# Performance work log

Measured on AMD Instinct MI355X. Metric: run time of the kernel, lower is better.

Reference implementation:

```python
import jax, jax.numpy as jnp
import numpy as np

HIDDEN = 2048
NUM_HEADS = 16
HEAD_SIZE = HIDDEN // NUM_HEADS  # 128
SEQ = 2048
BATCH = 2


def alibi_causal_bias(seq_len: int, num_heads: int) -> jnp.ndarray:
    """[1, H, S, S] bias: -(i-j)*slope for j<=i, -inf for j>i (per source mask)."""
    i = jnp.arange(seq_len)[:, None]
    j = jnp.arange(seq_len)[None, :]
    dist = -(i - j).astype(jnp.float32)            # 0 on diag, -(i-j) below
    causal = jnp.where(j > i, -jnp.inf, 0.0)
    base = jnp.where(j > i, 0.0, dist) + causal     # [S, S]
    if num_heads <= 8:
        slopes = jnp.asarray([1.0 / 2**k for k in range(num_heads)], jnp.float32)
    else:
        slopes = jnp.asarray([1.0 / 2**(k / 2) for k in range(num_heads)], jnp.float32)
    # NOTE: source multiplies the mask (including -inf part) by the slope;
    # -inf * positive slope is still -inf, so applying slopes to the finite
    # part and adding -inf causal term is equivalent.
    return slopes[None, :, None, None] * dist[None, None] * (j <= i)[None, None] + causal[None, None]


def setup_inputs() -> dict:
    key = jax.random.key(0)
    ks = jax.random.split(key, 3)
    sd = 1.0 / np.sqrt(HIDDEN)
    return {
        "x": jax.random.normal(ks[0], (BATCH, SEQ, HIDDEN), jnp.float32),
        "Wqkv": jax.random.normal(ks[1], (HIDDEN, 3 * HIDDEN), jnp.float32) * sd,
        "bqkv": jnp.zeros((3 * HIDDEN,), jnp.float32),
        "Wo": jax.random.normal(ks[2], (HIDDEN, HIDDEN), jnp.float32) * sd,
        "bo": jnp.zeros((HIDDEN,), jnp.float32),
    }


def reference(x, Wqkv, bqkv, Wo, bo):
    b, s, h = x.shape
    scale = 1.0 / np.sqrt(HEAD_SIZE)
    qkv = x @ Wqkv + bqkv                                   # [b, s, 3h]
    q, k, v = jnp.split(qkv, 3, axis=-1)
    def heads(t):
        return t.reshape(b, s, NUM_HEADS, HEAD_SIZE).transpose(0, 2, 1, 3)
    q, k, v = heads(q), heads(k), heads(v)                  # [b, H, s, d]
    scores = jnp.einsum("bhid,bhjd->bhij", q, k) * scale
    scores = scores + alibi_causal_bias(s, NUM_HEADS)
    attn = jax.nn.softmax(scores, axis=-1)                  # dropout=0 (eval)
    out = jnp.einsum("bhij,bhjd->bhid", attn, v)            # [b, H, s, d]
    out = out.transpose(0, 2, 1, 3).reshape(b, s, NUM_HEADS * HEAD_SIZE)
    return out @ Wo + bo
```

## Files before the change

kernel.cpp:

```cpp
#include <hip/hip_runtime.h>

typedef __attribute__((ext_vector_type(4))) float f32x4;
typedef __attribute__((ext_vector_type(8))) __bf16 bf16x8;
typedef unsigned short u16;

#define GAS(p) ((const __attribute__((address_space(1))) void*)(p))
#define LAS(p) ((__attribute__((address_space(3))) void*)(p))

__device__ __forceinline__ u16 f32_to_bf16(float f) {
  unsigned u = __builtin_bit_cast(unsigned, f);
  u += 0x7FFFu + ((u >> 16) & 1u);
  return (u16)(u >> 16);
}

__global__ __launch_bounds__(256) void k_convert(const float* __restrict__ X,
                                                 u16* __restrict__ Y, int n4) {
  int i = blockIdx.x * 256 + threadIdx.x;
  if (i >= n4) return;
  float4 v = ((const float4*)X)[i];
  ushort4 r;
  r.x = f32_to_bf16(v.x); r.y = f32_to_bf16(v.y);
  r.z = f32_to_bf16(v.z); r.w = f32_to_bf16(v.w);
  ((ushort4*)Y)[i] = r;
}

__global__ __launch_bounds__(256) void k_transpose_w(const float* __restrict__ W,
                                                     u16* __restrict__ WT,
                                                     int K, int N) {
  __shared__ float tile[32][33];
  int n0 = blockIdx.x * 32, k0 = blockIdx.y * 32;
  int tx = threadIdx.x & 31, ty = threadIdx.x >> 5;
#pragma unroll
  for (int r = 0; r < 4; ++r)
    tile[ty + r * 8][tx] = W[(long)(k0 + ty + r * 8) * N + n0 + tx];
  __syncthreads();
#pragma unroll
  for (int r = 0; r < 4; ++r)
    WT[(long)(n0 + ty + r * 8) * K + k0 + tx] = f32_to_bf16(tile[tx][ty + r * 8]);
}

__global__ __launch_bounds__(256) void k_transpose_v(const u16* __restrict__ V,
                                                     u16* __restrict__ VT) {
  __shared__ u16 tile[32][34];
  int s0 = blockIdx.x * 32, d0 = blockIdx.y * 32, bh = blockIdx.z;
  int tx = threadIdx.x & 31, ty = threadIdx.x >> 5;
  const u16* Vb = V + (long)bh * 2048 * 128;
  u16* VTb = VT + (long)bh * 128 * 2048;
#pragma unroll
  for (int r = 0; r < 4; ++r)
    tile[ty + r * 8][tx] = Vb[(long)(s0 + ty + r * 8) * 128 + d0 + tx];
  __syncthreads();
#pragma unroll
  for (int r = 0; r < 4; ++r)
    VTb[(long)(d0 + ty + r * 8) * 2048 + s0 + tx] = tile[tx][ty + r * 8];
}

template <int EPI>
__global__ __launch_bounds__(512, 2) void k_gemm(
    const u16* __restrict__ A, const u16* __restrict__ BT,
    const float* __restrict__ bias,
    u16* __restrict__ Qo, u16* __restrict__ Ko, u16* __restrict__ Vo,
    float* __restrict__ Cout, int M, int N, int K) {
  __shared__ alignas(16) u16 AS[3][128 * 64];
  __shared__ alignas(16) u16 BS[3][256 * 64];
  const int wave = threadIdx.x >> 6, lane = threadIdx.x & 63;
  const int wr = wave >> 2, wc = wave & 3;
  const int l15 = lane & 15, l4 = lane >> 4;
  const int sl = lane & 7, sr = (lane >> 3) & 7;

  const int nwg = gridDim.x;
  const int swz = ((int)blockIdx.x & 7) * (nwg >> 3) + ((int)blockIdx.x >> 3);
  const int mt = M >> 7;
  const int bm = swz % mt, bn = swz / mt;
  const int brow = bm * 128, bcol = bn * 256;
  const int NT = K >> 6;

  const u16* aBase = A + (long)(brow + wave * 8 + sr) * K + (sl ^ sr) * 8;
  const u16* bBase = BT + (long)(bcol + wave * 8 + sr) * K + (sl ^ sr) * 8;
  const long K64 = (long)K * 64;

  auto stage = [&](int t, int buf) {
    const long t64 = (long)t * 64;
#pragma unroll
    for (int j = 0; j < 2; ++j)
      __builtin_amdgcn_global_load_lds(GAS(aBase + t64 + j * K64),
                                       LAS(&AS[buf][(wave + j * 8) * 512]), 16, 0, 0);
#pragma unroll
    for (int j = 0; j < 4; ++j)
      __builtin_amdgcn_global_load_lds(GAS(bBase + t64 + j * K64),
                                       LAS(&BS[buf][(wave + j * 8) * 512]), 16, 0, 0);
  };

  const f32x4 fzero = {0.f, 0.f, 0.f, 0.f};
  f32x4 acc[4][4];
#pragma unroll
  for (int m = 0; m < 4; ++m)
#pragma unroll
    for (int n = 0; n < 4; ++n) acc[m][n] = fzero;

  auto compute = [&](int buf) {
    const u16* Ac = &AS[buf][0];
    const u16* Bc = &BS[buf][0];
    bf16x8 afr[4][2], bfr[4][2];
#pragma unroll
    for (int f = 0; f < 4; ++f)
#pragma unroll
      for (int kk = 0; kk < 2; ++kk) {
        const int Ra = wr * 64 + f * 16 + l15;
        afr[f][kk] =
            *(const bf16x8*)(Ac + Ra * 64 + (((kk * 4 + l4) ^ (l15 & 7)) * 8));
        const int Rb = wc * 64 + f * 16 + l15;
        bfr[f][kk] =
            *(const bf16x8*)(Bc + Rb * 64 + (((kk * 4 + l4) ^ (l15 & 7)) * 8));
      }
    __builtin_amdgcn_s_setprio(1);
#pragma unroll
    for (int m = 0; m < 4; ++m)
#pragma unroll
      for (int n = 0; n < 4; ++n)
#pragma unroll
        for (int kk = 0; kk < 2; ++kk)
          acc[m][n] = __builtin_amdgcn_mfma_f32_16x16x32_bf16(
              afr[m][kk], bfr[n][kk], acc[m][n], 0, 0, 0);
    __builtin_amdgcn_s_setprio(0);
  };

  stage(0, 0);
  stage(1, 1);
  int bufc = 0;
  for (int t = 0; t < NT - 1; ++t) {
    asm volatile("s_waitcnt vmcnt(6)" ::: "memory");
    __builtin_amdgcn_s_barrier();
    if (t + 2 < NT) {
      int bufn = bufc + 2;
      if (bufn >= 3) bufn -= 3;
      stage(t + 2, bufn);
    }
    compute(bufc);
    ++bufc;
    if (bufc == 3) bufc = 0;
  }
  asm volatile("s_waitcnt vmcnt(0)" ::: "memory");
  __builtin_amdgcn_s_barrier();
  compute(bufc);

  if (EPI == 0) {
#pragma unroll
    for (int n = 0; n < 4; ++n) {
      const int col = bcol + wc * 64 + n * 16 + l15;
      const int which = col >> 11;
      u16* dst = (which == 0) ? Qo : (which == 1) ? Ko : Vo;
      const int cc = col & 2047;
      const int h = cc >> 7, d = cc & 127;
      const float bv = bias[col];
#pragma unroll
      for (int m = 0; m < 4; ++m) {
#pragma unroll
        for (int r = 0; r < 4; ++r) {
          const int row = brow + wr * 64 + m * 16 + l4 * 4 + r;
          const int bb = row >> 11, s = row & 2047;
          dst[(((long)(bb * 16 + h)) * 2048 + s) * 128 + d] =
              f32_to_bf16(acc[m][n][r] + bv);
        }
      }
    }
  } else {
#pragma unroll
    for (int m = 0; m < 4; ++m)
#pragma unroll
      for (int r = 0; r < 4; ++r) {
        const int row = brow + wr * 64 + m * 16 + l4 * 4 + r;
#pragma unroll
        for (int n = 0; n < 4; ++n) {
          const int col = bcol + wc * 64 + n * 16 + l15;
          Cout[(long)row * N + col] = acc[m][n][r] + bias[col];
        }
      }
  }
}

__global__ __launch_bounds__(256, 4) void k_attn(const u16* __restrict__ Q,
                                                 const u16* __restrict__ Kp,
                                                 const u16* __restrict__ VT,
                                                 u16* __restrict__ Oa) {
  __shared__ alignas(16) u16 Kl[2][64 * 128];
  __shared__ alignas(16) u16 Vl[2][128 * 64];
  __shared__ alignas(16) u16 Pl[4][16 * 64];
  const int b = blockIdx.x;
  const int bh = b & 31;
  const int qt = 31 - (b >> 5);
  const int bb = bh >> 4, h = bh & 15;
  const int wave = threadIdx.x >> 6, lane = threadIdx.x & 63;
  const int l15 = lane & 15, l4 = lane >> 4;
  const int l7 = lane & 7, l8 = lane >> 3;
  const float LOG2E = 1.4426950408889634f;
  const float scale = 0.08838834764831845f * LOG2E;
  const float slope = exp2f(-0.5f * (float)h) * LOG2E;

  const int q0 = qt * 64 + wave * 16;
  const u16* Qb = Q + ((long)bh * 2048 + q0 + l15) * 128;
  bf16x8 qf[4];
#pragma unroll
  for (int kk = 0; kk < 4; ++kk) qf[kk] = *(const bf16x8*)(Qb + kk * 32 + l4 * 8);

  const u16* Kb = Kp + (long)bh * 2048 * 128;
  const u16* VTb = VT + (long)bh * 128 * 2048;

  auto stageK = [&](int jt, int buf) {
#pragma unroll
    for (int g = 0; g < 4; ++g) {
      const int wcc = g * 4 + wave;
      const int row = wcc * 4 + l4;
      const u16* src = Kb + (long)(jt * 64 + row) * 128 + ((l15 ^ (row & 7)) * 8);
      __builtin_amdgcn_global_load_lds(GAS(src), LAS(&Kl[buf][wcc * 512]), 16, 0, 0);
    }
  };
  auto stageV = [&](int jt, int buf) {
#pragma unroll
    for (int g = 0; g < 4; ++g) {
      const int wcc = g * 4 + wave;
      const int d = wcc * 8 + l8;
      const u16* src = VTb + (long)d * 2048 + jt * 64 + ((l7 ^ l8) * 8);
      __builtin_amdgcn_global_load_lds(GAS(src), LAS(&Vl[buf][wcc * 512]), 16, 0, 0);
    }
  };

  float rs[4];
  f32x4 O[8];
  const f32x4 fzero = {0.f, 0.f, 0.f, 0.f};
#pragma unroll
  for (int r = 0; r < 4; ++r) rs[r] = 0.f;
#pragma unroll
  for (int nb = 0; nb < 8; ++nb) O[nb] = fzero;

  u16* Pw = Pl[wave];
  const int irow = q0 + l4 * 4;
  const int sw = l15 & 7;

  stageK(0, 0);
  stageV(0, 0);
  __syncthreads();

  for (int jt = 0; jt <= qt; ++jt) {
    const int cur = jt & 1;
    if (jt < qt) {
      stageK(jt + 1, cur ^ 1);
      stageV(jt + 1, cur ^ 1);
    }
    const u16* Kc = Kl[cur];
    const u16* Vc = Vl[cur];
    const int j0 = jt * 64;
#pragma unroll
    for (int cb = 0; cb < 4; ++cb) {
      f32x4 sa = fzero;
      const u16* kp = Kc + (cb * 16 + l15) * 128;
#pragma unroll
      for (int kk = 0; kk < 4; ++kk) {
        bf16x8 kf = *(const bf16x8*)(kp + (((kk * 4 + l4) ^ sw) * 8));
        sa = __builtin_amdgcn_mfma_f32_16x16x32_bf16(qf[kk], kf, sa, 0, 0, 0);
      }
      const int j = j0 + cb * 16 + l15;
#pragma unroll
      for (int r = 0; r < 4; ++r) {
        int i = irow + r;
        float s = sa[r] * scale - slope * (float)(i - j);
        float p = __builtin_amdgcn_exp2f((j <= i) ? s : -1e30f);
        rs[r] += p;
        int rloc = l4 * 4 + r;
        int cbyte = (cb * 16 + l15) * 2;
        *(u16*)((char*)Pw + rloc * 128 + (cbyte ^ ((rloc & 7) << 4))) =
            f32_to_bf16(p);
      }
    }
    bf16x8 pf0 = *(const bf16x8*)((char*)Pw + l15 * 128 +
                                  ((l4 * 16) ^ ((l15 & 7) << 4)));
    bf16x8 pf1 = *(const bf16x8*)((char*)Pw + l15 * 128 +
                                  ((64 + l4 * 16) ^ ((l15 & 7) << 4)));
#pragma unroll
    for (int nb = 0; nb < 8; ++nb) {
      const u16* vp = Vc + (nb * 16 + l15) * 64;
      bf16x8 v0 = *(const bf16x8*)(vp + ((l4 ^ sw) * 8));
      bf16x8 v1 = *(const bf16x8*)(vp + (((4 + l4) ^ sw) * 8));
      O[nb] = __builtin_amdgcn_mfma_f32_16x16x32_bf16(pf0, v0, O[nb], 0, 0, 0);
      O[nb] = __builtin_amdgcn_mfma_f32_16x16x32_bf16(pf1, v1, O[nb], 0, 0, 0);
    }
    __syncthreads();
  }
#pragma unroll
  for (int r = 0; r < 4; ++r) {
    float v = rs[r];
    v += __shfl_xor(v, 1);
    v += __shfl_xor(v, 2);
    v += __shfl_xor(v, 4);
    v += __shfl_xor(v, 8);
    float inv = 1.f / v;
    int i = irow + r;
    u16* op = Oa + ((long)bb * 2048 + i) * 2048 + h * 128;
#pragma unroll
    for (int nb = 0; nb < 8; ++nb) op[nb * 16 + l15] = f32_to_bf16(O[nb][r] * inv);
  }
}

extern "C" void kernel_launch(void* const* d_in, const int* in_sizes, int n_in,
                              void* d_out, int out_size, void* d_ws, size_t ws_size,
                              hipStream_t stream) {
  const float* x = (const float*)d_in[0];
  const float* Wqkv = (const float*)d_in[1];
  const float* bqkv = (const float*)d_in[2];
  const float* Wo = (const float*)d_in[3];
  const float* bo = (const float*)d_in[4];
  float* out = (float*)d_out;

  char* ws = (char*)d_ws;
  u16* xb = (u16*)(ws);
  u16* VTb = (u16*)(ws);
  u16* WqkvT = (u16*)(ws + 16777216);
  u16* attn_out = (u16*)(ws + 16777216);
  u16* WoT = (u16*)(ws + 16777216 + 25165824);
  u16* Qb = (u16*)(ws + 50331648);
  u16* Kb = (u16*)(ws + 67108864);
  u16* Vb = (u16*)(ws + 83886080);

  k_convert<<<8192, 256, 0, stream>>>(x, xb, 8388608 / 4);
  k_transpose_w<<<dim3(192, 64), 256, 0, stream>>>(Wqkv, WqkvT, 2048, 6144);
  k_transpose_w<<<dim3(64, 64), 256, 0, stream>>>(Wo, WoT, 2048, 2048);
  k_gemm<0><<<dim3(768), 512, 0, stream>>>(xb, WqkvT, bqkv, Qb, Kb, Vb,
                                           nullptr, 4096, 6144, 2048);
  k_transpose_v<<<dim3(64, 4, 32), 256, 0, stream>>>(Vb, VTb);
  k_attn<<<dim3(1024), 256, 0, stream>>>(Qb, Kb, VTb, attn_out);
  k_gemm<1><<<dim3(256), 512, 0, stream>>>(attn_out, WoT, bo, nullptr,
                                           nullptr, nullptr, out, 4096, 2048,
                                           2048);
}
```

Measured before the change: 292.2 us.

## Use 256x256 tiled GEMM with interleaved load/compute schedule for QKV projection

```diff
diff --git a/kernel.cpp b/kernel.cpp
--- a/kernel.cpp
+++ b/kernel.cpp
@@ -53,6 +53,179 @@
 #pragma unroll
   for (int r = 0; r < 4; ++r)
     VTb[(long)(d0 + ty + r * 8) * 2048 + s0 + tx] = tile[tx][ty + r * 8];
+}
+
+template <int EPI>
+__global__ __launch_bounds__(512, 2) void k_gemm256(
+    const u16* __restrict__ A, const u16* __restrict__ BT,
+    const float* __restrict__ bias,
+    u16* __restrict__ Qo, u16* __restrict__ Ko, u16* __restrict__ Vo,
+    float* __restrict__ Cout, int M, int N, int K) {
+  __shared__ alignas(16) u16 AS[2][256 * 64];
+  __shared__ alignas(16) u16 BS[2][256 * 64];
+  const int wave = threadIdx.x >> 6, lane = threadIdx.x & 63;
+  const int wr = wave >> 2, wc = wave & 3;
+  const int l15 = lane & 15, l4 = lane >> 4;
+  const int sl = lane & 7, sr = (lane >> 3) & 7;
+
+  const int nwg = gridDim.x;
+  const int swz = ((int)blockIdx.x & 7) * (nwg >> 3) + ((int)blockIdx.x >> 3);
+  const int mt = M >> 8;
+  const int bm = swz % mt, bn = swz / mt;
+  const int brow = bm * 256, bcol = bn * 256;
+  const int NT = K >> 6;
+
+  const u16* aBase = A + (long)(brow + wave * 8 + sr) * K + (sl ^ sr) * 8;
+  const u16* bBase = BT + (long)(bcol + wave * 8 + sr) * K + (sl ^ sr) * 8;
+  const long K64 = (long)K * 64;
+
+  auto ld = [&](const u16* g, u16* l) {
+    __builtin_amdgcn_global_load_lds(GAS(g), LAS(l + wave * 512), 16, 0, 0);
+  };
+  auto stA1 = [&](long t64, int buf) {
+    ld(aBase + t64, &AS[buf][0]);
+    ld(aBase + t64 + 2 * K64, &AS[buf][128 * 64]);
+  };
+  auto stA2 = [&](long t64, int buf) {
+    ld(aBase + t64 + K64, &AS[buf][64 * 64]);
+    ld(aBase + t64 + 3 * K64, &AS[buf][192 * 64]);
+  };
+  auto stB1 = [&](long t64, int buf) {
+    ld(bBase + t64, &BS[buf][0]);
+    ld(bBase + t64 + K64, &BS[buf][64 * 64]);
+  };
+  auto stB2 = [&](long t64, int buf) {
+    ld(bBase + t64 + 2 * K64, &BS[buf][128 * 64]);
+    ld(bBase + t64 + 3 * K64, &BS[buf][192 * 64]);
+  };
+
+  const f32x4 fzero = {0.f, 0.f, 0.f, 0.f};
+  f32x4 acc[8][4];
+#pragma unroll
+  for (int m = 0; m < 8; ++m)
+#pragma unroll
+    for (int n = 0; n < 4; ++n) acc[m][n] = fzero;
+
+  bf16x8 bfA[4][2], bfB[4][2], afA[2][2], afB[2][2];
+
+#define BAR()                      \
+  __builtin_amdgcn_s_barrier();    \
+  asm volatile("" ::: "memory")
+
+#define RD_A(DST, P, BUF)                                                   \
+  do {                                                                      \
+    _Pragma("unroll") for (int mm = 0; mm < 2; ++mm)                        \
+        _Pragma("unroll") for (int kk = 0; kk < 2; ++kk) {                  \
+      const int R = wr * 128 + ((P) * 2 + mm) * 16 + l15;                   \
+      DST[mm][kk] = *(const bf16x8*)(&AS[BUF][R * 64 +                      \
+                                             (((kk * 4 + l4) ^ (l15 & 7)) * 8)]); \
+    }                                                                       \
+  } while (0)
+
+#define RD_B(DST, BUF)                                                      \
+  do {                                                                      \
+    _Pragma("unroll") for (int n = 0; n < 4; ++n)                           \
+        _Pragma("unroll") for (int kk = 0; kk < 2; ++kk) {                  \
+      const int R = wc * 64 + n * 16 + l15;                                 \
+      DST[n][kk] = *(const bf16x8*)(&BS[BUF][R * 64 +                       \
+                                            (((kk * 4 + l4) ^ (l15 & 7)) * 8)]); \
+    }                                                                       \
+  } while (0)
+
+#define MM(P, AF, BF)                                                       \
+  do {                                                                      \
+    __builtin_amdgcn_s_setprio(1);                                          \
+    _Pragma("unroll") for (int mm = 0; mm < 2; ++mm)                        \
+        _Pragma("unroll") for (int n = 0; n < 4; ++n)                       \
+            _Pragma("unroll") for (int kk = 0; kk < 2; ++kk)                \
+                acc[(P) * 2 + mm][n] = __builtin_amdgcn_mfma_f32_16x16x32_bf16( \
+                    AF[mm][kk], BF[n][kk], acc[(P) * 2 + mm][n], 0, 0, 0);  \
+    __builtin_amdgcn_s_setprio(0);                                          \
+  } while (0)
+
+#define TILE(T, CUR, NXT, BFC, BFN)                                         \
+  do {                                                                      \
+    const bool pre = ((T) + 1 < NT);                                        \
+    const long n64 = (long)((T) + 1) * 64;                                  \
+     if (pre) stA1(n64, NXT);                                       \
+    BAR();                                                                  \
+    RD_A(afB, 1, CUR);                                                      \
+    MM(0, afA, BFC);                                                        \
+    BAR();                                                                  \
+     if (pre) stB1(n64, NXT);                                       \
+    if (pre)                                                                \
+      asm volatile("s_waitcnt vmcnt(4)" ::: "memory");                      \
+    else                                                                    \
+      asm volatile("s_waitcnt vmcnt(0)" ::: "memory");                      \
+    BAR();                                                                  \
+    RD_A(afA, 2, CUR);                                                      \
+    MM(1, afB, BFC);                                                        \
+    BAR();                                                                  \
+     if (pre) stB2(n64, NXT);                                       \
+    BAR();                                                                  \
+    RD_A(afB, 3, CUR);                                                      \
+    MM(2, afA, BFC);                                                        \
+    BAR();                                                                  \
+     if (pre) stA2(n64, NXT);                                       \
+    if (pre) asm volatile("s_waitcnt vmcnt(2)" ::: "memory");               \
+    BAR();                                                                  \
+    if (pre) {                                                              \
+      RD_B(BFN, NXT);                                                       \
+      RD_A(afA, 0, NXT);                                                    \
+    }                                                                       \
+    MM(3, afB, BFC);                                                        \
+    BAR();                                                                  \
+  } while (0)
+
+  stA1(0, 0); stB1(0, 0); stB2(0, 0); stA2(0, 0);
+  asm volatile("s_waitcnt vmcnt(0)" ::: "memory");
+  BAR();
+  RD_B(bfA, 0);
+  RD_A(afA, 0, 0);
+
+  for (int tp = 0; tp < NT; tp += 2) {
+    TILE(tp, 0, 1, bfA, bfB);
+    TILE(tp + 1, 1, 0, bfB, bfA);
+  }
+#undef TILE
+#undef MM
+#undef RD_B
+#undef RD_A
+#undef BAR
+
+  if (EPI == 0) {
+#pragma unroll
+    for (int n = 0; n < 4; ++n) {
+      const int col = bcol + wc * 64 + n * 16 + l15;
+      const int which = col >> 11;
+      u16* dst = (which == 0) ? Qo : (which == 1) ? Ko : Vo;
+      const int cc = col & 2047;
+      const int h = cc >> 7, d = cc & 127;
+      const float bv = bias[col];
+#pragma unroll
+      for (int m = 0; m < 8; ++m) {
+#pragma unroll
+        for (int r = 0; r < 4; ++r) {
+          const int row = brow + wr * 128 + m * 16 + l4 * 4 + r;
+          const int bb = row >> 11, s = row & 2047;
+          dst[(((long)(bb * 16 + h)) * 2048 + s) * 128 + d] =
+              f32_to_bf16(acc[m][n][r] + bv);
+        }
+      }
+    }
+  } else {
+#pragma unroll
+    for (int m = 0; m < 8; ++m)
+#pragma unroll
+      for (int r = 0; r < 4; ++r) {
+        const int row = brow + wr * 128 + m * 16 + l4 * 4 + r;
+#pragma unroll
+        for (int n = 0; n < 4; ++n) {
+          const int col = bcol + wc * 64 + n * 16 + l15;
+          Cout[(long)row * N + col] = acc[m][n][r] + bias[col];
+        }
+      }
+  }
 }
 
 template <int EPI>
@@ -324,8 +497,8 @@
   k_convert<<<8192, 256, 0, stream>>>(x, xb, 8388608 / 4);
   k_transpose_w<<<dim3(192, 64), 256, 0, stream>>>(Wqkv, WqkvT, 2048, 6144);
   k_transpose_w<<<dim3(64, 64), 256, 0, stream>>>(Wo, WoT, 2048, 2048);
-  k_gemm<0><<<dim3(768), 512, 0, stream>>>(xb, WqkvT, bqkv, Qb, Kb, Vb,
-                                           nullptr, 4096, 6144, 2048);
+  k_gemm256<0><<<dim3(384), 512, 0, stream>>>(xb, WqkvT, bqkv, Qb, Kb, Vb,
+                                              nullptr, 4096, 6144, 2048);
   k_transpose_v<<<dim3(64, 4, 32), 256, 0, stream>>>(Vb, VTb);
   k_attn<<<dim3(1024), 256, 0, stream>>>(Qb, Kb, VTb, attn_out);
   k_gemm<1><<<dim3(256), 512, 0, stream>>>(attn_out, WoT, bo, nullptr,
```

After: 288.4 us. About the same (-1.3%).

## Shrink GEMM tiles to 128x128x32 with 4 waves and more blocks

Applied to the files above, without the earlier changes.

```diff
diff --git a/kernel.cpp b/kernel.cpp
--- a/kernel.cpp
+++ b/kernel.cpp
@@ -56,39 +56,40 @@
 }
 
 template <int EPI>
-__global__ __launch_bounds__(512, 2) void k_gemm(
+__global__ __launch_bounds__(256, 3) void k_gemm(
     const u16* __restrict__ A, const u16* __restrict__ BT,
     const float* __restrict__ bias,
     u16* __restrict__ Qo, u16* __restrict__ Ko, u16* __restrict__ Vo,
     float* __restrict__ Cout, int M, int N, int K) {
-  __shared__ alignas(16) u16 AS[3][128 * 64];
-  __shared__ alignas(16) u16 BS[3][256 * 64];
+  __shared__ alignas(16) u16 AS[3][128 * 32];
+  __shared__ alignas(16) u16 BS[3][128 * 32];
   const int wave = threadIdx.x >> 6, lane = threadIdx.x & 63;
-  const int wr = wave >> 2, wc = wave & 3;
+  const int wr = wave >> 1, wc = wave & 1;
   const int l15 = lane & 15, l4 = lane >> 4;
-  const int sl = lane & 7, sr = (lane >> 3) & 7;
+  const int srow = lane >> 2;
+  const int sslot = (lane & 3) ^ (srow & 3);
 
   const int nwg = gridDim.x;
   const int swz = ((int)blockIdx.x & 7) * (nwg >> 3) + ((int)blockIdx.x >> 3);
   const int mt = M >> 7;
   const int bm = swz % mt, bn = swz / mt;
-  const int brow = bm * 128, bcol = bn * 256;
-  const int NT = K >> 6;
-
-  const u16* aBase = A + (long)(brow + wave * 8 + sr) * K + (sl ^ sr) * 8;
-  const u16* bBase = BT + (long)(bcol + wave * 8 + sr) * K + (sl ^ sr) * 8;
+  const int brow = bm * 128, bcol = bn * 128;
+  const int NT = K >> 5;
+
+  const u16* aBase = A + (long)(brow + wave * 16 + srow) * K + sslot * 8;
+  const u16* bBase = BT + (long)(bcol + wave * 16 + srow) * K + sslot * 8;
   const long K64 = (long)K * 64;
 
   auto stage = [&](int t, int buf) {
-    const long t64 = (long)t * 64;
-#pragma unroll
-    for (int j = 0; j < 2; ++j)
-      __builtin_amdgcn_global_load_lds(GAS(aBase + t64 + j * K64),
-                                       LAS(&AS[buf][(wave + j * 8) * 512]), 16, 0, 0);
-#pragma unroll
-    for (int j = 0; j < 4; ++j)
-      __builtin_amdgcn_global_load_lds(GAS(bBase + t64 + j * K64),
-                                       LAS(&BS[buf][(wave + j * 8) * 512]), 16, 0, 0);
+    const long t32 = (long)t * 32;
+    __builtin_amdgcn_global_load_lds(GAS(aBase + t32),
+                                     LAS(&AS[buf][wave * 512]), 16, 0, 0);
+    __builtin_amdgcn_global_load_lds(GAS(aBase + t32 + K64),
+                                     LAS(&AS[buf][(wave + 4) * 512]), 16, 0, 0);
+    __builtin_amdgcn_global_load_lds(GAS(bBase + t32),
+                                     LAS(&BS[buf][wave * 512]), 16, 0, 0);
+    __builtin_amdgcn_global_load_lds(GAS(bBase + t32 + K64),
+                                     LAS(&BS[buf][(wave + 4) * 512]), 16, 0, 0);
   };
 
   const f32x4 fzero = {0.f, 0.f, 0.f, 0.f};
@@ -101,27 +102,21 @@
   auto compute = [&](int buf) {
     const u16* Ac = &AS[buf][0];
     const u16* Bc = &BS[buf][0];
-    bf16x8 afr[4][2], bfr[4][2];
-#pragma unroll
-    for (int f = 0; f < 4; ++f)
-#pragma unroll
-      for (int kk = 0; kk < 2; ++kk) {
-        const int Ra = wr * 64 + f * 16 + l15;
-        afr[f][kk] =
-            *(const bf16x8*)(Ac + Ra * 64 + (((kk * 4 + l4) ^ (l15 & 7)) * 8));
-        const int Rb = wc * 64 + f * 16 + l15;
-        bfr[f][kk] =
-            *(const bf16x8*)(Bc + Rb * 64 + (((kk * 4 + l4) ^ (l15 & 7)) * 8));
-      }
+    bf16x8 afr[4], bfr[4];
+#pragma unroll
+    for (int f = 0; f < 4; ++f) {
+      const int Ra = wr * 64 + f * 16 + l15;
+      afr[f] = *(const bf16x8*)(Ac + Ra * 32 + ((l4 ^ (l15 & 3)) * 8));
+      const int Rb = wc * 64 + f * 16 + l15;
+      bfr[f] = *(const bf16x8*)(Bc + Rb * 32 + ((l4 ^ (l15 & 3)) * 8));
+    }
     __builtin_amdgcn_s_setprio(1);
 #pragma unroll
     for (int m = 0; m < 4; ++m)
 #pragma unroll
       for (int n = 0; n < 4; ++n)
-#pragma unroll
-        for (int kk = 0; kk < 2; ++kk)
-          acc[m][n] = __builtin_amdgcn_mfma_f32_16x16x32_bf16(
-              afr[m][kk], bfr[n][kk], acc[m][n], 0, 0, 0);
+        acc[m][n] = __builtin_amdgcn_mfma_f32_16x16x32_bf16(afr[m], bfr[n],
+                                                            acc[m][n], 0, 0, 0);
     __builtin_amdgcn_s_setprio(0);
   };
 
@@ -129,7 +124,7 @@
   stage(1, 1);
   int bufc = 0;
   for (int t = 0; t < NT - 1; ++t) {
-    asm volatile("s_waitcnt vmcnt(6)" ::: "memory");
+    asm volatile("s_waitcnt vmcnt(4)" ::: "memory");
     __builtin_amdgcn_s_barrier();
     if (t + 2 < NT) {
       int bufn = bufc + 2;
@@ -145,14 +140,14 @@
   compute(bufc);
 
   if (EPI == 0) {
+    const int which = bcol >> 11;
+    u16* dst = (which == 0) ? Qo : (which == 1) ? Ko : Vo;
+    const int cbase = bcol & 2047;
 #pragma unroll
     for (int n = 0; n < 4; ++n) {
-      const int col = bcol + wc * 64 + n * 16 + l15;
-      const int which = col >> 11;
-      u16* dst = (which == 0) ? Qo : (which == 1) ? Ko : Vo;
-      const int cc = col & 2047;
-      const int h = cc >> 7, d = cc & 127;
-      const float bv = bias[col];
+      const int col = cbase + wc * 64 + n * 16 + l15;
+      const int h = col >> 7, d = col & 127;
+      const float bv = bias[bcol + wc * 64 + n * 16 + l15];
 #pragma unroll
       for (int m = 0; m < 4; ++m) {
 #pragma unroll
@@ -324,11 +319,11 @@
   k_convert<<<8192, 256, 0, stream>>>(x, xb, 8388608 / 4);
   k_transpose_w<<<dim3(192, 64), 256, 0, stream>>>(Wqkv, WqkvT, 2048, 6144);
   k_transpose_w<<<dim3(64, 64), 256, 0, stream>>>(Wo, WoT, 2048, 2048);
-  k_gemm<0><<<dim3(768), 512, 0, stream>>>(xb, WqkvT, bqkv, Qb, Kb, Vb,
-                                           nullptr, 4096, 6144, 2048);
+  k_gemm<0><<<dim3(1536), 256, 0, stream>>>(xb, WqkvT, bqkv, Qb, Kb, Vb,
+                                            nullptr, 4096, 6144, 2048);
   k_transpose_v<<<dim3(64, 4, 32), 256, 0, stream>>>(Vb, VTb);
   k_attn<<<dim3(1024), 256, 0, stream>>>(Qb, Kb, VTb, attn_out);
-  k_gemm<1><<<dim3(256), 512, 0, stream>>>(attn_out, WoT, bo, nullptr,
+  k_gemm<1><<<dim3(512), 256, 0, stream>>>(attn_out, WoT, bo, nullptr,
                                            nullptr, nullptr, out, 4096, 2048,
                                            2048);
 }
```

Result: faster. 275.2 us (-5.8%).
